# Optimization experiments

Measured on AMD Instinct MI355X. Metric: run time of the kernel, lower is better.

## Reference

```python
import jax, jax.numpy as jnp
import numpy as np

B = 262144   # n_batch
DT = 0.01    # filter period T_filter from reset_state


def _quat_mul(q, r):
    # Hamilton product, q,r: [B,4] in (w,x,y,z)
    w1, x1, y1, z1 = q[:, 0], q[:, 1], q[:, 2], q[:, 3]
    w2, x2, y2, z2 = r[:, 0], r[:, 1], r[:, 2], r[:, 3]
    return jnp.stack([
        w1 * w2 - x1 * x2 - y1 * y2 - z1 * z2,
        w1 * x2 + x1 * w2 + y1 * z2 - z1 * y2,
        w1 * y2 - x1 * z2 + y1 * w2 + z1 * x2,
        w1 * z2 + x1 * y2 - y1 * x2 + z1 * w2,
    ], axis=-1)


def _inject(state, err):
    # state: [B,7,1] = [p(3); q(4)], err: [B,6,1] = [dp(3); dtheta(3)]
    p = state[:, :3, 0] + err[:, :3, 0]
    q = state[:, 3:, 0]
    dth = 0.5 * err[:, 3:, 0]
    dq = jnp.concatenate([jnp.ones_like(dth[:, :1]), dth], axis=-1)  # small-angle quat
    qn = _quat_mul(q, dq)
    qn = qn / jnp.linalg.norm(qn, axis=-1, keepdims=True)
    return jnp.concatenate([p, qn], axis=-1)[:, :, None]


def _Xdx(state):
    # ESKF Jacobian of nominal state wrt error state: [B,7,6]
    q = state[:, 3:, 0]
    bsz = q.shape[0]
    w, xq, y, z = q[:, 0], q[:, 1], q[:, 2], q[:, 3]
    Qd = 0.5 * jnp.stack([
        jnp.stack([-xq, -y, -z], -1),
        jnp.stack([w, -z, y], -1),
        jnp.stack([z, w, -xq], -1),
        jnp.stack([-y, xq, w], -1),
    ], axis=1)  # [B,4,3]
    I3 = jnp.broadcast_to(jnp.eye(3, dtype=state.dtype), (bsz, 3, 3))
    top = jnp.concatenate([I3, jnp.zeros((bsz, 3, 3), state.dtype)], axis=-1)
    bot = jnp.concatenate([jnp.zeros((bsz, 4, 3), state.dtype), Qd], axis=-1)
    return jnp.concatenate([top, bot], axis=1)


def setup_inputs() -> dict:
    key = jax.random.key(0)
    k1, k2, k3 = jax.random.split(key, 3)
    x = jax.random.normal(k1, (14, B), dtype=jnp.float32)
    p = jax.random.normal(k2, (B, 3), dtype=jnp.float32)
    q = jax.random.normal(k3, (B, 4), dtype=jnp.float32)
    q = q / jnp.linalg.norm(q, axis=-1, keepdims=True)
    state = jnp.concatenate([p, q], axis=-1)[:, :, None]  # [B,7,1]
    # covariances as in reset_state (diagonal, batched)
    covariance = jnp.tile(jnp.diag(jnp.array([1e-3] * 3 + [0.2] * 3, jnp.float32))[None], (B, 1, 1))
    Q = jnp.tile(jnp.diag(jnp.array([1e-4] * 3 + [2e-4] * 3, jnp.float32))[None], (B, 1, 1))
    R = jnp.tile(jnp.diag(jnp.array([1e-6] * 3 + [1e-4] * 4, jnp.float32))[None], (B, 1, 1))
    return {"x": x, "state": state, "covariance": covariance, "Q": Q, "R": R}


def reference(x, state, covariance, Q, R):
    # --- unpack forward args (mirrors forward(): permute(2,1,0)) ---
    twist = x[8:14].T[:, :, None]        # [B,6,1] control
    measurement = x[0:7].T[:, :, None]   # [B,7,1]
    # --- predict: F = I6, B_matrix = dt * I6 ---
    error_state_prior = DT * twist                       # B_matrix @ u
    predict_state = _inject(state, error_state_prior)    # [B,7,1]
    P = covariance + Q                                   # F P F^T + Q with F = I
    # --- update ---
    H = _Xdx(state)                                      # Hx = I7, so H = Xdx: [B,7,6]
    Ht = jnp.swapaxes(H, 1, 2)                           # [B,6,7]
    S = H @ P @ Ht + R                                   # [B,7,7]
    K = P @ Ht @ jnp.linalg.inv(S)                       # [B,6,7]
    innovation = measurement - predict_state             # [B,7,1]
    error_state = K @ innovation                         # [B,6,1]
    I6 = jnp.eye(6, dtype=P.dtype)
    P_new = (I6[None] - K @ H) @ P                       # stored as self.covariance (side effect)
    new_state = _inject(predict_state, error_state)      # [B,7,1]
    del P_new  # forward() returns only the state
    return new_state
```

## Files before the change

kernel.cpp:

```cpp
#include <hip/hip_runtime.h>

#define DT_C 0.01f

__device__ __forceinline__ void gload_lds16(const float* g, float* l) {
    __builtin_amdgcn_global_load_lds(
        (const __attribute__((address_space(1))) void*)g,
        (__attribute__((address_space(3))) void*)l,
        16, 0, 0);
}

__global__ __launch_bounds__(64, 2) void eskf_kernel(
    const float* __restrict__ x,
    const float* __restrict__ state,
    const float* __restrict__ cov,
    const float* __restrict__ Qm,
    const float* __restrict__ Rm,
    float* __restrict__ out,
    int B)
{
    __shared__ float ldsC[64 * 36];
    __shared__ float ldsQ[64 * 36];
    __shared__ float ldsR[64 * 49];
    __shared__ float ldsS[64 * 7];

    const int lane = threadIdx.x;
    const int eb   = blockIdx.x * 64;
    const int b    = eb + lane;

    {
        const float* gc = cov + (size_t)eb * 36;
#pragma unroll
        for (int k = 0; k < 9; ++k)
            gload_lds16(gc + 4 * (k * 64 + lane), ldsC + 4 * (k * 64 + lane));

        const float* gq = Qm + (size_t)eb * 36;
#pragma unroll
        for (int k = 0; k < 9; ++k)
            gload_lds16(gq + 4 * (k * 64 + lane), ldsQ + 4 * (k * 64 + lane));

        const float* gr = Rm + (size_t)eb * 49;
#pragma unroll
        for (int k = 0; k < 12; ++k)
            gload_lds16(gr + 4 * (k * 64 + lane), ldsR + 4 * (k * 64 + lane));
        if (lane < 16)
            gload_lds16(gr + 4 * (768 + lane), ldsR + 4 * (768 + lane));

        const float* gs = state + (size_t)eb * 7;
        gload_lds16(gs + 4 * lane, ldsS + 4 * lane);
        if (lane < 48)
            gload_lds16(gs + 4 * (64 + lane), ldsS + 4 * (64 + lane));
    }

    float meas[7], tw[6];
#pragma unroll
    for (int i = 0; i < 7; ++i) meas[i] = x[i * B + b];
#pragma unroll
    for (int i = 0; i < 6; ++i) tw[i] = x[(8 + i) * B + b];

    asm volatile("s_waitcnt vmcnt(0)" ::: "memory");

    float P[36];
    {
        const float4* c4 = (const float4*)(ldsC + lane * 36);
        const float4* q4 = (const float4*)(ldsQ + lane * 36);
#pragma unroll
        for (int i = 0; i < 9; ++i) {
            float4 a = c4[i], bb = q4[i];
            P[4 * i + 0] = a.x + bb.x;
            P[4 * i + 1] = a.y + bb.y;
            P[4 * i + 2] = a.z + bb.z;
            P[4 * i + 3] = a.w + bb.w;
        }
    }

    float st[7];
    {
        const float* ls = ldsS + lane * 7;
#pragma unroll
        for (int i = 0; i < 7; ++i) st[i] = ls[i];
    }

    float S[7][7];
    {
        const float* lr = ldsR + lane * 49;
#pragma unroll
        for (int i = 0; i < 7; ++i)
#pragma unroll
            for (int j = 0; j < 7; ++j) S[i][j] = lr[i * 7 + j];
    }

    float ps[7];
    {
        float d0 = 0.5f * DT_C * tw[3], d1 = 0.5f * DT_C * tw[4], d2 = 0.5f * DT_C * tw[5];
        ps[0] = st[0] + DT_C * tw[0];
        ps[1] = st[1] + DT_C * tw[1];
        ps[2] = st[2] + DT_C * tw[2];
        float w = st[3], xx = st[4], yy = st[5], zz = st[6];
        float qw = w - xx * d0 - yy * d1 - zz * d2;
        float qx = w * d0 + xx + yy * d2 - zz * d1;
        float qy = w * d1 - xx * d2 + yy + zz * d0;
        float qz = w * d2 + xx * d1 - yy * d0 + zz;
        float inv = rsqrtf(qw * qw + qx * qx + qy * qy + qz * qz);
        ps[3] = qw * inv; ps[4] = qx * inv; ps[5] = qy * inv; ps[6] = qz * inv;
    }

    float Qd[4][3];
    {
        float w = st[3], xx = st[4], yy = st[5], zz = st[6];
        Qd[0][0] = -0.5f * xx; Qd[0][1] = -0.5f * yy; Qd[0][2] = -0.5f * zz;
        Qd[1][0] =  0.5f * w;  Qd[1][1] = -0.5f * zz; Qd[1][2] =  0.5f * yy;
        Qd[2][0] =  0.5f * zz; Qd[2][1] =  0.5f * w;  Qd[2][2] = -0.5f * xx;
        Qd[3][0] = -0.5f * yy; Qd[3][1] =  0.5f * xx; Qd[3][2] =  0.5f * w;
    }

#pragma unroll
    for (int i = 0; i < 3; ++i)
#pragma unroll
        for (int j = 0; j < 3; ++j)
            S[i][j] += P[i * 6 + j];

    float T[4][6];
#pragma unroll
    for (int i = 0; i < 4; ++i)
#pragma unroll
        for (int c = 0; c < 6; ++c) {
            float acc = 0.f;
#pragma unroll
            for (int k = 0; k < 3; ++k) acc += Qd[i][k] * P[(3 + k) * 6 + c];
            T[i][c] = acc;
        }

#pragma unroll
    for (int i = 0; i < 4; ++i)
#pragma unroll
        for (int j = 0; j < 3; ++j) S[3 + i][j] += T[i][j];

#pragma unroll
    for (int i = 0; i < 3; ++i)
#pragma unroll
        for (int j = 0; j < 4; ++j) {
            float acc = 0.f;
#pragma unroll
            for (int k = 0; k < 3; ++k) acc += P[i * 6 + 3 + k] * Qd[j][k];
            S[i][3 + j] += acc;
        }

#pragma unroll
    for (int i = 0; i < 4; ++i)
#pragma unroll
        for (int j = 0; j < 4; ++j) {
            float acc = 0.f;
#pragma unroll
            for (int l = 0; l < 3; ++l) acc += T[i][3 + l] * Qd[j][l];
            S[3 + i][3 + j] += acc;
        }

    float y[7];
#pragma unroll
    for (int i = 0; i < 7; ++i) y[i] = meas[i] - ps[i];

#pragma unroll
    for (int k = 0; k < 7; ++k) {
        float inv = 1.0f / S[k][k];
#pragma unroll
        for (int i = k + 1; i < 7; ++i) {
            float f = S[i][k] * inv;
#pragma unroll
            for (int j = k + 1; j < 7; ++j) S[i][j] -= f * S[k][j];
            y[i] -= f * y[k];
        }
    }
#pragma unroll
    for (int k = 6; k >= 0; --k) {
        float acc = y[k];
#pragma unroll
        for (int j = k + 1; j < 7; ++j) acc -= S[k][j] * y[j];
        y[k] = acc / S[k][k];
    }

    float z6[6];
    z6[0] = y[0]; z6[1] = y[1]; z6[2] = y[2];
#pragma unroll
    for (int c = 0; c < 3; ++c) {
        float acc = 0.f;
#pragma unroll
        for (int i = 0; i < 4; ++i) acc += Qd[i][c] * y[3 + i];
        z6[3 + c] = acc;
    }
    float es[6];
#pragma unroll
    for (int i = 0; i < 6; ++i) {
        float acc = 0.f;
#pragma unroll
        for (int j = 0; j < 6; ++j) acc += P[i * 6 + j] * z6[j];
        es[i] = acc;
    }

    float o0 = ps[0] + es[0];
    float o1 = ps[1] + es[1];
    float o2 = ps[2] + es[2];
    float d0 = 0.5f * es[3], d1 = 0.5f * es[4], d2 = 0.5f * es[5];
    float w = ps[3], xx = ps[4], yy = ps[5], zz = ps[6];
    float qw = w - xx * d0 - yy * d1 - zz * d2;
    float qx = w * d0 + xx + yy * d2 - zz * d1;
    float qy = w * d1 - xx * d2 + yy + zz * d0;
    float qz = w * d2 + xx * d1 - yy * d0 + zz;
    float inv = rsqrtf(qw * qw + qx * qx + qy * qy + qz * qz);

    {
        float* ol = ldsS + lane * 7;
        ol[0] = o0; ol[1] = o1; ol[2] = o2;
        ol[3] = qw * inv; ol[4] = qx * inv; ol[5] = qy * inv; ol[6] = qz * inv;
        asm volatile("s_waitcnt lgkmcnt(0)" ::: "memory");

        float4*       og = (float4*)(out + (size_t)eb * 7);
        const float4* lf = (const float4*)ldsS;
        og[lane] = lf[lane];
        if (lane < 48) og[64 + lane] = lf[64 + lane];
    }
}

extern "C" void kernel_launch(void* const* d_in, const int* in_sizes, int n_in,
                              void* d_out, int out_size, void* d_ws, size_t ws_size,
                              hipStream_t stream) {
    const float* x     = (const float*)d_in[0];
    const float* state = (const float*)d_in[1];
    const float* cov   = (const float*)d_in[2];
    const float* Qm    = (const float*)d_in[3];
    const float* Rm    = (const float*)d_in[4];
    float* out = (float*)d_out;
    int B = in_sizes[1] / 7;
    int grid = B / 64;
    eskf_kernel<<<grid, 64, 0, stream>>>(x, state, cov, Qm, Rm, out, B);
}
```

Baseline: 167.7 us.

## Double-buffer async LDS staging across eight groups per persistent block

Each block now processes eight 64-element groups, double-buffering all inputs (including x, now also staged via global_load_lds) in shared memory so the loads for group g+2 are issued while group g computes. Explicit vmcnt waits order the buffers. The aim is to hide global memory latency behind compute instead of relying on occupancy. In exchange the grid shrinks eightfold and each block uses much more LDS, which reduces the number of resident waves. The hand-tuned vmcnt counts are fragile and depend on the exact number of outstanding loads and stores.

```diff
diff --git a/kernel.cpp b/kernel.cpp
--- a/kernel.cpp
+++ b/kernel.cpp
@@ -1,6 +1,8 @@
 #include <hip/hip_runtime.h>
 
 #define DT_C 0.01f
+#define WAITVM(n)  asm volatile("s_waitcnt vmcnt(" #n ")" ::: "memory")
+#define WAITLGKM0  asm volatile("s_waitcnt lgkmcnt(0)" ::: "memory")
 
 __device__ __forceinline__ void gload_lds16(const float* g, float* l) {
     __builtin_amdgcn_global_load_lds(
@@ -9,7 +11,16 @@
         16, 0, 0);
 }
 
-__global__ __launch_bounds__(64, 2) void eskf_kernel(
+#define OFF_X   0
+#define OFF_C   896
+#define OFF_Q   3200
+#define OFF_R   5504
+#define OFF_ST  8640
+#define BUFDW   9088
+#define OFF_OUT (2*BUFDW)
+#define GPW     8
+
+__global__ __launch_bounds__(64) void eskf_kernel(
     const float* __restrict__ x,
     const float* __restrict__ state,
     const float* __restrict__ cov,
@@ -18,205 +29,231 @@
     float* __restrict__ out,
     int B)
 {
-    __shared__ float ldsC[64 * 36];
-    __shared__ float ldsQ[64 * 36];
-    __shared__ float ldsR[64 * 49];
-    __shared__ float ldsS[64 * 7];
-
-    const int lane = threadIdx.x;
-    const int eb   = blockIdx.x * 64;
-    const int b    = eb + lane;
-
-    {
+    __shared__ float lds[2 * BUFDW + 448];
+    const int lane  = threadIdx.x;
+    const int gbase = blockIdx.x * GPW;
+
+    auto STAGE = [&](int g, float* Lb) {
+        const int eb = (gbase + g) * 64;
+        {
+            const int r0 = lane >> 4;
+            const int c0 = (lane & 15) * 4;
+            const float* gx = x + (size_t)eb + c0;
+            float* lx = Lb + OFF_X;
+            gload_lds16(gx + (size_t)(0  + r0) * B, lx +   0 + 4 * lane);
+            gload_lds16(gx + (size_t)(4  + r0) * B, lx + 256 + 4 * lane);
+            gload_lds16(gx + (size_t)(8  + r0) * B, lx + 512 + 4 * lane);
+            if (lane < 32)
+                gload_lds16(gx + (size_t)(12 + r0) * B, lx + 768 + 4 * lane);
+        }
         const float* gc = cov + (size_t)eb * 36;
+        float* lc = Lb + OFF_C;
 #pragma unroll
         for (int k = 0; k < 9; ++k)
-            gload_lds16(gc + 4 * (k * 64 + lane), ldsC + 4 * (k * 64 + lane));
+            gload_lds16(gc + 4 * (k * 64 + lane), lc + 4 * (k * 64 + lane));
 
         const float* gq = Qm + (size_t)eb * 36;
+        float* lq = Lb + OFF_Q;
 #pragma unroll
         for (int k = 0; k < 9; ++k)
-            gload_lds16(gq + 4 * (k * 64 + lane), ldsQ + 4 * (k * 64 + lane));
+            gload_lds16(gq + 4 * (k * 64 + lane), lq + 4 * (k * 64 + lane));
 
         const float* gr = Rm + (size_t)eb * 49;
+        float* lr = Lb + OFF_R;
 #pragma unroll
         for (int k = 0; k < 12; ++k)
-            gload_lds16(gr + 4 * (k * 64 + lane), ldsR + 4 * (k * 64 + lane));
+            gload_lds16(gr + 4 * (k * 64 + lane), lr + 4 * (k * 64 + lane));
         if (lane < 16)
-            gload_lds16(gr + 4 * (768 + lane), ldsR + 4 * (768 + lane));
+            gload_lds16(gr + 4 * (768 + lane), lr + 4 * (768 + lane));
 
         const float* gs = state + (size_t)eb * 7;
-        gload_lds16(gs + 4 * lane, ldsS + 4 * lane);
+        float* lst = Lb + OFF_ST;
+        gload_lds16(gs + 4 * lane, lst + 4 * lane);
         if (lane < 48)
-            gload_lds16(gs + 4 * (64 + lane), ldsS + 4 * (64 + lane));
-    }
-
-    float meas[7], tw[6];
-#pragma unroll
-    for (int i = 0; i < 7; ++i) meas[i] = x[i * B + b];
-#pragma unroll
-    for (int i = 0; i < 6; ++i) tw[i] = x[(8 + i) * B + b];
-
-    asm volatile("s_waitcnt vmcnt(0)" ::: "memory");
-
-    float P[36];
-    {
-        const float4* c4 = (const float4*)(ldsC + lane * 36);
-        const float4* q4 = (const float4*)(ldsQ + lane * 36);
-#pragma unroll
-        for (int i = 0; i < 9; ++i) {
-            float4 a = c4[i], bb = q4[i];
-            P[4 * i + 0] = a.x + bb.x;
-            P[4 * i + 1] = a.y + bb.y;
-            P[4 * i + 2] = a.z + bb.z;
-            P[4 * i + 3] = a.w + bb.w;
-        }
-    }
-
-    float st[7];
-    {
-        const float* ls = ldsS + lane * 7;
-#pragma unroll
-        for (int i = 0; i < 7; ++i) st[i] = ls[i];
-    }
-
-    float S[7][7];
-    {
-        const float* lr = ldsR + lane * 49;
-#pragma unroll
-        for (int i = 0; i < 7; ++i)
-#pragma unroll
-            for (int j = 0; j < 7; ++j) S[i][j] = lr[i * 7 + j];
-    }
-
-    float ps[7];
-    {
-        float d0 = 0.5f * DT_C * tw[3], d1 = 0.5f * DT_C * tw[4], d2 = 0.5f * DT_C * tw[5];
-        ps[0] = st[0] + DT_C * tw[0];
-        ps[1] = st[1] + DT_C * tw[1];
-        ps[2] = st[2] + DT_C * tw[2];
-        float w = st[3], xx = st[4], yy = st[5], zz = st[6];
+            gload_lds16(gs + 4 * (64 + lane), lst + 4 * (64 + lane));
+    };
+
+    auto PHASE = [&](int g, float* Lb, bool dostage) {
+        float meas[7], tw[6];
+#pragma unroll
+        for (int i = 0; i < 7; ++i) meas[i] = Lb[OFF_X + i * 64 + lane];
+#pragma unroll
+        for (int i = 0; i < 6; ++i) tw[i]  = Lb[OFF_X + (8 + i) * 64 + lane];
+
+        float P[36];
+        {
+            const float4* c4 = (const float4*)(Lb + OFF_C + lane * 36);
+            const float4* q4 = (const float4*)(Lb + OFF_Q + lane * 36);
+#pragma unroll
+            for (int i = 0; i < 9; ++i) {
+                float4 a = c4[i], bq = q4[i];
+                P[4 * i + 0] = a.x + bq.x;
+                P[4 * i + 1] = a.y + bq.y;
+                P[4 * i + 2] = a.z + bq.z;
+                P[4 * i + 3] = a.w + bq.w;
+            }
+        }
+        float st[7];
+        {
+            const float* ls = Lb + OFF_ST + lane * 7;
+#pragma unroll
+            for (int i = 0; i < 7; ++i) st[i] = ls[i];
+        }
+        float S[7][7];
+        {
+            const float* lr = Lb + OFF_R + lane * 49;
+#pragma unroll
+            for (int i = 0; i < 7; ++i)
+#pragma unroll
+                for (int j = 0; j < 7; ++j) S[i][j] = lr[i * 7 + j];
+        }
+
+        WAITLGKM0;
+        if (dostage) STAGE(g + 2, Lb);
+
+        float ps[7];
+        {
+            float d0 = 0.5f * DT_C * tw[3], d1 = 0.5f * DT_C * tw[4], d2 = 0.5f * DT_C * tw[5];
+            ps[0] = st[0] + DT_C * tw[0];
+            ps[1] = st[1] + DT_C * tw[1];
+            ps[2] = st[2] + DT_C * tw[2];
+            float w = st[3], xx = st[4], yy = st[5], zz = st[6];
+            float qw = w - xx * d0 - yy * d1 - zz * d2;
+            float qx = w * d0 + xx + yy * d2 - zz * d1;
+            float qy = w * d1 - xx * d2 + yy + zz * d0;
+            float qz = w * d2 + xx * d1 - yy * d0 + zz;
+            float inv = rsqrtf(qw * qw + qx * qx + qy * qy + qz * qz);
+            ps[3] = qw * inv; ps[4] = qx * inv; ps[5] = qy * inv; ps[6] = qz * inv;
+        }
+
+        float Qd[4][3];
+        {
+            float w = st[3], xx = st[4], yy = st[5], zz = st[6];
+            Qd[0][0] = -0.5f * xx; Qd[0][1] = -0.5f * yy; Qd[0][2] = -0.5f * zz;
+            Qd[1][0] =  0.5f * w;  Qd[1][1] = -0.5f * zz; Qd[1][2] =  0.5f * yy;
+            Qd[2][0] =  0.5f * zz; Qd[2][1] =  0.5f * w;  Qd[2][2] = -0.5f * xx;
+            Qd[3][0] = -0.5f * yy; Qd[3][1] =  0.5f * xx; Qd[3][2] =  0.5f * w;
+        }
+
+#pragma unroll
+        for (int i = 0; i < 3; ++i)
+#pragma unroll
+            for (int j = 0; j < 3; ++j) S[i][j] += P[i * 6 + j];
+
+        float T[4][6];
+#pragma unroll
+        for (int i = 0; i < 4; ++i)
+#pragma unroll
+            for (int c = 0; c < 6; ++c) {
+                float acc = 0.f;
+#pragma unroll
+                for (int k = 0; k < 3; ++k) acc += Qd[i][k] * P[(3 + k) * 6 + c];
+                T[i][c] = acc;
+            }
+#pragma unroll
+        for (int i = 0; i < 4; ++i)
+#pragma unroll
+            for (int j = 0; j < 3; ++j) S[3 + i][j] += T[i][j];
+#pragma unroll
+        for (int i = 0; i < 3; ++i)
+#pragma unroll
+            for (int j = 0; j < 4; ++j) {
+                float acc = 0.f;
+#pragma unroll
+                for (int k = 0; k < 3; ++k) acc += P[i * 6 + 3 + k] * Qd[j][k];
+                S[i][3 + j] += acc;
+            }
+#pragma unroll
+        for (int i = 0; i < 4; ++i)
+#pragma unroll
+            for (int j = 0; j < 4; ++j) {
+                float acc = 0.f;
+#pragma unroll
+                for (int l = 0; l < 3; ++l) acc += T[i][3 + l] * Qd[j][l];
+                S[3 + i][3 + j] += acc;
+            }
+
+        float y[7];
+#pragma unroll
+        for (int i = 0; i < 7; ++i) y[i] = meas[i] - ps[i];
+
+#pragma unroll
+        for (int k = 0; k < 7; ++k) {
+            float inv = 1.0f / S[k][k];
+#pragma unroll
+            for (int i = k + 1; i < 7; ++i) {
+                float f = S[i][k] * inv;
+#pragma unroll
+                for (int j = k + 1; j < 7; ++j) S[i][j] -= f * S[k][j];
+                y[i] -= f * y[k];
+            }
+        }
+#pragma unroll
+        for (int k = 6; k >= 0; --k) {
+            float acc = y[k];
+#pragma unroll
+            for (int j = k + 1; j < 7; ++j) acc -= S[k][j] * y[j];
+            y[k] = acc / S[k][k];
+        }
+
+        float z6[6];
+        z6[0] = y[0]; z6[1] = y[1]; z6[2] = y[2];
+#pragma unroll
+        for (int c = 0; c < 3; ++c) {
+            float acc = 0.f;
+#pragma unroll
+            for (int i = 0; i < 4; ++i) acc += Qd[i][c] * y[3 + i];
+            z6[3 + c] = acc;
+        }
+        float es[6];
+#pragma unroll
+        for (int i = 0; i < 6; ++i) {
+            float acc = 0.f;
+#pragma unroll
+            for (int j = 0; j < 6; ++j) acc += P[i * 6 + j] * z6[j];
+            es[i] = acc;
+        }
+
+        float o0 = ps[0] + es[0];
+        float o1 = ps[1] + es[1];
+        float o2 = ps[2] + es[2];
+        float d0 = 0.5f * es[3], d1 = 0.5f * es[4], d2 = 0.5f * es[5];
+        float w = ps[3], xx = ps[4], yy = ps[5], zz = ps[6];
         float qw = w - xx * d0 - yy * d1 - zz * d2;
         float qx = w * d0 + xx + yy * d2 - zz * d1;
         float qy = w * d1 - xx * d2 + yy + zz * d0;
         float qz = w * d2 + xx * d1 - yy * d0 + zz;
         float inv = rsqrtf(qw * qw + qx * qx + qy * qy + qz * qz);
-        ps[3] = qw * inv; ps[4] = qx * inv; ps[5] = qy * inv; ps[6] = qz * inv;
-    }
-
-    float Qd[4][3];
-    {
-        float w = st[3], xx = st[4], yy = st[5], zz = st[6];
-        Qd[0][0] = -0.5f * xx; Qd[0][1] = -0.5f * yy; Qd[0][2] = -0.5f * zz;
-        Qd[1][0] =  0.5f * w;  Qd[1][1] = -0.5f * zz; Qd[1][2] =  0.5f * yy;
-        Qd[2][0] =  0.5f * zz; Qd[2][1] =  0.5f * w;  Qd[2][2] = -0.5f * xx;
-        Qd[3][0] = -0.5f * yy; Qd[3][1] =  0.5f * xx; Qd[3][2] =  0.5f * w;
-    }
-
-#pragma unroll
-    for (int i = 0; i < 3; ++i)
-#pragma unroll
-        for (int j = 0; j < 3; ++j)
-            S[i][j] += P[i * 6 + j];
-
-    float T[4][6];
-#pragma unroll
-    for (int i = 0; i < 4; ++i)
-#pragma unroll
-        for (int c = 0; c < 6; ++c) {
-            float acc = 0.f;
-#pragma unroll
-            for (int k = 0; k < 3; ++k) acc += Qd[i][k] * P[(3 + k) * 6 + c];
-            T[i][c] = acc;
-        }
-
-#pragma unroll
-    for (int i = 0; i < 4; ++i)
-#pragma unroll
-        for (int j = 0; j < 3; ++j) S[3 + i][j] += T[i][j];
-
-#pragma unroll
-    for (int i = 0; i < 3; ++i)
-#pragma unroll
-        for (int j = 0; j < 4; ++j) {
-            float acc = 0.f;
-#pragma unroll
-            for (int k = 0; k < 3; ++k) acc += P[i * 6 + 3 + k] * Qd[j][k];
-            S[i][3 + j] += acc;
-        }
-
-#pragma unroll
-    for (int i = 0; i < 4; ++i)
-#pragma unroll
-        for (int j = 0; j < 4; ++j) {
-            float acc = 0.f;
-#pragma unroll
-            for (int l = 0; l < 3; ++l) acc += T[i][3 + l] * Qd[j][l];
-            S[3 + i][3 + j] += acc;
-        }
-
-    float y[7];
-#pragma unroll
-    for (int i = 0; i < 7; ++i) y[i] = meas[i] - ps[i];
-
-#pragma unroll
-    for (int k = 0; k < 7; ++k) {
-        float inv = 1.0f / S[k][k];
-#pragma unroll
-        for (int i = k + 1; i < 7; ++i) {
-            float f = S[i][k] * inv;
-#pragma unroll
-            for (int j = k + 1; j < 7; ++j) S[i][j] -= f * S[k][j];
-            y[i] -= f * y[k];
-        }
-    }
-#pragma unroll
-    for (int k = 6; k >= 0; --k) {
-        float acc = y[k];
-#pragma unroll
-        for (int j = k + 1; j < 7; ++j) acc -= S[k][j] * y[j];
-        y[k] = acc / S[k][k];
-    }
-
-    float z6[6];
-    z6[0] = y[0]; z6[1] = y[1]; z6[2] = y[2];
-#pragma unroll
-    for (int c = 0; c < 3; ++c) {
-        float acc = 0.f;
-#pragma unroll
-        for (int i = 0; i < 4; ++i) acc += Qd[i][c] * y[3 + i];
-        z6[3 + c] = acc;
-    }
-    float es[6];
-#pragma unroll
-    for (int i = 0; i < 6; ++i) {
-        float acc = 0.f;
-#pragma unroll
-        for (int j = 0; j < 6; ++j) acc += P[i * 6 + j] * z6[j];
-        es[i] = acc;
-    }
-
-    float o0 = ps[0] + es[0];
-    float o1 = ps[1] + es[1];
-    float o2 = ps[2] + es[2];
-    float d0 = 0.5f * es[3], d1 = 0.5f * es[4], d2 = 0.5f * es[5];
-    float w = ps[3], xx = ps[4], yy = ps[5], zz = ps[6];
-    float qw = w - xx * d0 - yy * d1 - zz * d2;
-    float qx = w * d0 + xx + yy * d2 - zz * d1;
-    float qy = w * d1 - xx * d2 + yy + zz * d0;
-    float qz = w * d2 + xx * d1 - yy * d0 + zz;
-    float inv = rsqrtf(qw * qw + qx * qx + qy * qy + qz * qz);
-
-    {
-        float* ol = ldsS + lane * 7;
-        ol[0] = o0; ol[1] = o1; ol[2] = o2;
-        ol[3] = qw * inv; ol[4] = qx * inv; ol[5] = qy * inv; ol[6] = qz * inv;
-        asm volatile("s_waitcnt lgkmcnt(0)" ::: "memory");
-
-        float4*       og = (float4*)(out + (size_t)eb * 7);
-        const float4* lf = (const float4*)ldsS;
-        og[lane] = lf[lane];
-        if (lane < 48) og[64 + lane] = lf[64 + lane];
+
+        {
+            float* ol = lds + OFF_OUT + lane * 7;
+            ol[0] = o0; ol[1] = o1; ol[2] = o2;
+            ol[3] = qw * inv; ol[4] = qx * inv; ol[5] = qy * inv; ol[6] = qz * inv;
+            WAITLGKM0;
+            float4*       og = (float4*)(out + (size_t)(gbase + g) * 64 * 7);
+            const float4* lf = (const float4*)(lds + OFF_OUT);
+            og[lane] = lf[lane];
+            if (lane < 48) og[64 + lane] = lf[64 + lane];
+        }
+    };
+
+    float* L0 = lds;
+    float* L1 = lds + BUFDW;
+
+    STAGE(0, L0);
+    STAGE(1, L1);
+
+    for (int p = 0; p < 4; ++p) {
+        bool more = (p < 3);
+        WAITVM(37);
+        PHASE(2 * p, L0, more);
+        if (more) {
+            WAITVM(37);
+            PHASE(2 * p + 1, L1, true);
+        } else {
+            WAITVM(4);
+            PHASE(7, L1, false);
+        }
     }
 }
 
@@ -230,6 +267,6 @@
     const float* Rm    = (const float*)d_in[4];
     float* out = (float*)d_out;
     int B = in_sizes[1] / 7;
-    int grid = B / 64;
+    int grid = B / (GPW * 64);
     eskf_kernel<<<grid, 64, 0, stream>>>(x, state, cov, Qm, Rm, out, B);
 }
```

After: 173.6 us. 1.04x slower.
